# Optimization experiments

Hardware: AMD Instinct MI355X
Metric: run time of the kernel (lower is better)

## Reference

```python
import jax, jax.numpy as jnp
import numpy as np

N = 100000
E = 640000
D = 128

def setup_inputs() -> dict:
    key = jax.random.key(0)
    ks = jax.random.split(key, 12)
    s = 1.0 / np.sqrt(D)
    inp = {
        'x': jax.random.normal(ks[0], (N, D), dtype=jnp.float32),
        'edge_index': jax.random.randint(ks[1], (2, E), 0, N, dtype=jnp.int64),
    }
    names = ['W1l', 'b1', 'W1r', 'W2l', 'b2', 'W2r', 'W3l', 'b3', 'W3r']
    shapes = [(D, D), (D,), (D, D), (D, D), (D,), (D, D), (D, D), (D,), (D, D)]
    for i, (n, sh) in enumerate(zip(names, shapes)):
        inp[n] = jax.random.normal(ks[2 + i], sh, dtype=jnp.float32) * s
    return inp

def _sage_conv(x, src, dst, Wl, b, Wr):
    # mean aggregation of source features at destination nodes
    msg = x[src]                                            # [E, D] gather
    agg = jax.ops.segment_sum(msg, dst, num_segments=N)     # [N, D]
    cnt = jax.ops.segment_sum(jnp.ones((src.shape[0],), x.dtype), dst, num_segments=N)
    agg = agg / jnp.maximum(cnt, 1.0)[:, None]
    # lin_l(aggr) + lin_r(x); bias lives in lin_l (PyG default)
    return agg @ Wl.T + b + x @ Wr.T

def reference(x, edge_index, W1l, b1, W1r, W2l, b2, W2r, W3l, b3, W3r):
    src, dst = edge_index[0], edge_index[1]
    h = jax.nn.relu(_sage_conv(x, src, dst, W1l, b1, W1r))
    # dropout layers are identity in eval mode
    h = jax.nn.relu(_sage_conv(h, src, dst, W2l, b2, W2r))
    h = _sage_conv(h, src, dst, W3l, b3, W3r)
    return h
```

## Files before the change

### kernel.cpp

```cpp
#include <hip/hip_runtime.h>


typedef __attribute__((ext_vector_type(8))) short bf16x8;
typedef __attribute__((ext_vector_type(4))) float f32x4;
typedef __attribute__((ext_vector_type(4))) unsigned int u32x4;

__device__ __forceinline__ unsigned short f2bf(float f) {
  unsigned u = __float_as_uint(f);
  u += 0x7fffu + ((u >> 16) & 1u);
  return (unsigned short)(u >> 16);
}

__global__ __launch_bounds__(256) void cvt_kernel(const float* __restrict__ in,
                                                  unsigned short* __restrict__ out, int n8) {
  int i = blockIdx.x * 256 + threadIdx.x;
  if (i >= n8) return;
  const float4* p = (const float4*)(in + (size_t)i * 8);
  float4 a = p[0], b = p[1];
  union { unsigned short s[8]; u32x4 u; } pk;
  pk.s[0] = f2bf(a.x); pk.s[1] = f2bf(a.y); pk.s[2] = f2bf(a.z); pk.s[3] = f2bf(a.w);
  pk.s[4] = f2bf(b.x); pk.s[5] = f2bf(b.y); pk.s[6] = f2bf(b.z); pk.s[7] = f2bf(b.w);
  *(u32x4*)(out + (size_t)i * 8) = pk.u;
}

__global__ __launch_bounds__(256) void count_kernel(const int* __restrict__ dst,
                                                    int* __restrict__ cnt, int E, float pscale) {
  int p = blockIdx.x & 7;
  int blk = blockIdx.x >> 3;
  int stride = (gridDim.x >> 3) * 256;
  for (int e = blk * 256 + threadIdx.x; e < E; e += stride) {
    int d = dst[e];
    int pd = (int)((float)d * pscale);
    pd = pd > 7 ? 7 : pd;
    if (pd == p) atomicAdd(&cnt[d], 1);
  }
}

__global__ __launch_bounds__(256) void partial_kernel(const int* __restrict__ cnt,
                                                      int* __restrict__ blocksum, int N) {
  __shared__ int red[256];
  int t = threadIdx.x;
  int idx = blockIdx.x * 2048 + t * 8;
  int s = 0;
  if (idx + 8 <= N) {
    int4 a = *(const int4*)(cnt + idx);
    int4 b = *(const int4*)(cnt + idx + 4);
    s = a.x + a.y + a.z + a.w + b.x + b.y + b.z + b.w;
  } else {
    for (int i = idx; i < N && i < idx + 8; ++i) s += cnt[i];
  }
  red[t] = s;
  __syncthreads();
  for (int off = 128; off > 0; off >>= 1) {
    if (t < off) red[t] += red[t + off];
    __syncthreads();
  }
  if (t == 0) blocksum[blockIdx.x] = red[0];
}

__global__ __launch_bounds__(64) void scanmid_kernel(const int* __restrict__ blocksum,
                                                     int* __restrict__ blockoff, int nb) {
  int l = threadIdx.x;
  int own = (l < nb) ? blocksum[l] : 0;
  int v = own;
  for (int off = 1; off < 64; off <<= 1) {
    int u = __shfl_up(v, off);
    if (l >= off) v += u;
  }
  if (l < nb) blockoff[l] = v - own;
}

__global__ __launch_bounds__(256) void final_kernel(const int* __restrict__ cnt,
                                                    const int* __restrict__ blockoff,
                                                    int* __restrict__ rowstart,
                                                    int* __restrict__ cursor,
                                                    float* __restrict__ inv, int N) {
  __shared__ int thr[256];
  int t = threadIdx.x;
  int idx = blockIdx.x * 2048 + t * 8;
  int c[8];
  int s = 0;
#pragma unroll
  for (int i = 0; i < 8; ++i) {
    int n = idx + i;
    c[i] = (n < N) ? cnt[n] : 0;
    s += c[i];
  }
  thr[t] = s;
  __syncthreads();
  for (int off = 1; off < 256; off <<= 1) {
    int u = (t >= off) ? thr[t - off] : 0;
    __syncthreads();
    thr[t] += u;
    __syncthreads();
  }
  int run = blockoff[blockIdx.x] + thr[t] - s;
#pragma unroll
  for (int i = 0; i < 8; ++i) {
    int n = idx + i;
    if (n < N) {
      rowstart[n] = run;
      cursor[n] = run;
      inv[n] = 1.f / fmaxf((float)c[i], 1.f);
      run += c[i];
      if (n == N - 1) rowstart[N] = run;
    }
  }
}

__global__ __launch_bounds__(256) void fill_kernel(const int* __restrict__ src,
                                                   const int* __restrict__ dst,
                                                   int* __restrict__ cursor,
                                                   int* __restrict__ elist, int E, float pscale) {
  int p = blockIdx.x & 7;
  int blk = blockIdx.x >> 3;
  int stride = (gridDim.x >> 3) * 256;
  for (int e = blk * 256 + threadIdx.x; e < E; e += stride) {
    int d = dst[e];
    int s = src[e];
    int pd = (int)((float)d * pscale);
    pd = pd > 7 ? 7 : pd;
    if (pd == p) {
      int pos = atomicAdd(&cursor[d], 1);
      elist[pos] = s;
    }
  }
}

__global__ __launch_bounds__(256) void aggregate_kernel(const unsigned short* __restrict__ xbf,
                                                        const int* __restrict__ rowstart,
                                                        const int* __restrict__ elist,
                                                        const float* __restrict__ inv,
                                                        unsigned short* __restrict__ aggbf, int N) {
  int gid = blockIdx.x * 256 + threadIdx.x;
  int node = gid >> 4;
  if (node >= N) return;
  int l16 = threadIdx.x & 15;

  int beg = rowstart[node], end = rowstart[node + 1];
  float acc[8];
#pragma unroll
  for (int j = 0; j < 8; ++j) acc[j] = 0.f;

  int e = beg;
  for (; e + 2 <= end; e += 2) {
    int s0 = elist[e];
    int s1 = elist[e + 1];
    u32x4 u0 = *(const u32x4*)(xbf + ((size_t)s0 << 7) + l16 * 8);
    u32x4 u1 = *(const u32x4*)(xbf + ((size_t)s1 << 7) + l16 * 8);
#pragma unroll
    for (int d = 0; d < 4; ++d) {
      acc[2 * d]     += __uint_as_float(u0[d] << 16);
      acc[2 * d + 1] += __uint_as_float(u0[d] & 0xffff0000u);
      acc[2 * d]     += __uint_as_float(u1[d] << 16);
      acc[2 * d + 1] += __uint_as_float(u1[d] & 0xffff0000u);
    }
  }
  if (e < end) {
    int s0 = elist[e];
    u32x4 u0 = *(const u32x4*)(xbf + ((size_t)s0 << 7) + l16 * 8);
#pragma unroll
    for (int d = 0; d < 4; ++d) {
      acc[2 * d]     += __uint_as_float(u0[d] << 16);
      acc[2 * d + 1] += __uint_as_float(u0[d] & 0xffff0000u);
    }
  }

  float iv = inv[node];
  union { unsigned short s[8]; u32x4 u; } pk;
#pragma unroll
  for (int j = 0; j < 8; ++j) pk.s[j] = f2bf(acc[j] * iv);
  *(u32x4*)(aggbf + ((size_t)node << 7) + l16 * 8) = pk.u;
}

__global__ __launch_bounds__(256, 2) void sage_gemm(
    const unsigned short* __restrict__ Abf, const unsigned short* __restrict__ Xbf,
    const float* __restrict__ Wl, const float* __restrict__ Wr, const float* __restrict__ bias,
    float* __restrict__ outf, unsigned short* __restrict__ outb, int N, int relu) {
  __shared__ __align__(16) unsigned short sW[2][128][128];
  const int tid = threadIdx.x;
  for (int it = tid; it < 4096; it += 256) {
    int m = it >> 11;
    int o = (it >> 4) & 127;
    int ch = it & 15;
    const float* wsrc = (m ? Wr : Wl) + o * 128 + ch * 8;
    float4 f0 = *(const float4*)wsrc;
    float4 f1 = *(const float4*)(wsrc + 4);
    union { unsigned short s[8]; u32x4 u; } pk;
    pk.s[0] = f2bf(f0.x); pk.s[1] = f2bf(f0.y); pk.s[2] = f2bf(f0.z); pk.s[3] = f2bf(f0.w);
    pk.s[4] = f2bf(f1.x); pk.s[5] = f2bf(f1.y); pk.s[6] = f2bf(f1.z); pk.s[7] = f2bf(f1.w);
    *(u32x4*)&sW[m][o][(ch ^ (o & 15)) << 3] = pk.u;
  }
  __syncthreads();

  const int l = tid & 63;
  const int w = tid >> 6;
  const int l15 = l & 15;
  const int lg = l >> 4;
  const int row_base = blockIdx.x * 256 + w * 64;

  f32x4 acc[4][8];
#pragma unroll
  for (int rt = 0; rt < 4; ++rt)
#pragma unroll
    for (int ot = 0; ot < 8; ++ot) acc[rt][ot] = f32x4{0.f, 0.f, 0.f, 0.f};

  union frag { u32x4 u; bf16x8 v; };

  int rrow[4];
#pragma unroll
  for (int rt = 0; rt < 4; ++rt) {
    int r = row_base + rt * 16 + l15;
    rrow[rt] = (r < N) ? r : (N - 1);
  }

#pragma unroll
  for (int h = 0; h < 2; ++h) {
    const unsigned short* Asrc = h ? Xbf : Abf;
#pragma unroll
    for (int ks = 0; ks < 4; ++ks) {
      frag af[4];
#pragma unroll
      for (int rt = 0; rt < 4; ++rt)
        af[rt].u = *(const u32x4*)(Asrc + ((size_t)rrow[rt] << 7) + (ks * 32 + lg * 8));
      frag bq[8];
#pragma unroll
      for (int ot = 0; ot < 8; ++ot)
        bq[ot].u = *(const u32x4*)&sW[h][ot * 16 + l15][((((ks << 2) | lg) ^ l15)) << 3];
#pragma unroll
      for (int rt = 0; rt < 4; ++rt)
#pragma unroll
        for (int ot = 0; ot < 8; ++ot)
          acc[rt][ot] = __builtin_amdgcn_mfma_f32_16x16x32_bf16(af[rt].v, bq[ot].v, acc[rt][ot], 0, 0, 0);
    }
  }

  float bv[8];
#pragma unroll
  for (int ot = 0; ot < 8; ++ot) bv[ot] = bias[ot * 16 + l15];

#pragma unroll
  for (int rt = 0; rt < 4; ++rt) {
#pragma unroll
    for (int i = 0; i < 4; ++i) {
      int r = row_base + rt * 16 + lg * 4 + i;
      if (r < N) {
#pragma unroll
        for (int ot = 0; ot < 8; ++ot) {
          float v = acc[rt][ot][i] + bv[ot];
          if (relu) v = fmaxf(v, 0.f);
          size_t idx = ((size_t)r << 7) + ot * 16 + l15;
          if (outf) outf[idx] = v;
          else outb[idx] = f2bf(v);
        }
      }
    }
  }
}

extern "C" void kernel_launch(void* const* d_in, const int* in_sizes, int n_in,
                              void* d_out, int out_size, void* d_ws, size_t ws_size,
                              hipStream_t stream) {
  (void)n_in; (void)out_size; (void)ws_size;
  const float* x = (const float*)d_in[0];
  const int* ei = (const int*)d_in[1];
  const float* W1l = (const float*)d_in[2];
  const float* b1 = (const float*)d_in[3];
  const float* W1r = (const float*)d_in[4];
  const float* W2l = (const float*)d_in[5];
  const float* b2 = (const float*)d_in[6];
  const float* W2r = (const float*)d_in[7];
  const float* W3l = (const float*)d_in[8];
  const float* b3 = (const float*)d_in[9];
  const float* W3r = (const float*)d_in[10];
  float* out = (float*)d_out;

  const int N = in_sizes[0] / 128;
  const int E = in_sizes[1] / 2;
  const int* srcp = ei;
  const int* dstp = ei + E;
  const float pscale = 8.0f / (float)N;

  char* ws = (char*)d_ws;
  size_t off = 0;
  auto alloc = [&](size_t bytes) {
    void* p = ws + off;
    off = (off + bytes + 255) & ~(size_t)255;
    return p;
  };
  unsigned short* bufA = (unsigned short*)alloc((size_t)N * 128 * 2);
  unsigned short* bufB = (unsigned short*)alloc((size_t)N * 128 * 2);
  unsigned short* aggbf = (unsigned short*)alloc((size_t)N * 128 * 2);
  int* cnt = (int*)alloc((size_t)N * 4);
  int* rowstart = (int*)alloc((size_t)(N + 1) * 4);
  int* cursor = (int*)alloc((size_t)N * 4);
  float* inv = (float*)alloc((size_t)N * 4);
  int* elist = (int*)alloc((size_t)E * 4);
  int* blocksum = (int*)alloc(64 * 4);
  int* blockoff = (int*)alloc(64 * 4);

  const int nb = (N + 2047) / 2048;

  hipMemsetAsync(cnt, 0, (size_t)N * 4, stream);
  cvt_kernel<<<(N * 128 / 8 + 255) / 256, 256, 0, stream>>>(x, bufA, N * 128 / 8);
  count_kernel<<<1024, 256, 0, stream>>>(dstp, cnt, E, pscale);
  partial_kernel<<<nb, 256, 0, stream>>>(cnt, blocksum, N);
  scanmid_kernel<<<1, 64, 0, stream>>>(blocksum, blockoff, nb);
  final_kernel<<<nb, 256, 0, stream>>>(cnt, blockoff, rowstart, cursor, inv, N);
  fill_kernel<<<1024, 256, 0, stream>>>(srcp, dstp, cursor, elist, E, pscale);

  int aggBlocks = (N * 16 + 255) / 256;
  int gemmBlocks = (N + 255) / 256;

  aggregate_kernel<<<aggBlocks, 256, 0, stream>>>(bufA, rowstart, elist, inv, aggbf, N);
  sage_gemm<<<gemmBlocks, 256, 0, stream>>>(aggbf, bufA, W1l, W1r, b1, nullptr, bufB, N, 1);
  aggregate_kernel<<<aggBlocks, 256, 0, stream>>>(bufB, rowstart, elist, inv, aggbf, N);
  sage_gemm<<<gemmBlocks, 256, 0, stream>>>(aggbf, bufB, W2l, W2r, b2, nullptr, bufA, N, 1);
  aggregate_kernel<<<aggBlocks, 256, 0, stream>>>(bufA, rowstart, elist, inv, aggbf, N);
  sage_gemm<<<gemmBlocks, 256, 0, stream>>>(aggbf, bufA, W3l, W3r, b3, out, nullptr, N, 0);
}
```

Measured before the change: 358.4 us.

## Pre-convert weights to bf16 once and shrink GEMM tiles, reading weights from global

```diff
diff --git a/kernel.cpp b/kernel.cpp
--- a/kernel.cpp
+++ b/kernel.cpp
@@ -21,6 +21,26 @@
   pk.s[0] = f2bf(a.x); pk.s[1] = f2bf(a.y); pk.s[2] = f2bf(a.z); pk.s[3] = f2bf(a.w);
   pk.s[4] = f2bf(b.x); pk.s[5] = f2bf(b.y); pk.s[6] = f2bf(b.z); pk.s[7] = f2bf(b.w);
   *(u32x4*)(out + (size_t)i * 8) = pk.u;
+}
+
+__global__ __launch_bounds__(256) void wcvt_kernel(const float* __restrict__ w0, const float* __restrict__ w1,
+                                                   const float* __restrict__ w2, const float* __restrict__ w3,
+                                                   const float* __restrict__ w4, const float* __restrict__ w5,
+                                                   unsigned short* __restrict__ out) {
+  int i = blockIdx.x * 256 + threadIdx.x;
+  int m = i >> 11;
+  int off = (i & 2047) * 8;
+  const float* src;
+  switch (m) {
+    case 0: src = w0; break; case 1: src = w1; break; case 2: src = w2; break;
+    case 3: src = w3; break; case 4: src = w4; break; default: src = w5; break;
+  }
+  float4 a = *(const float4*)(src + off);
+  float4 b = *(const float4*)(src + off + 4);
+  union { unsigned short s[8]; u32x4 u; } pk;
+  pk.s[0] = f2bf(a.x); pk.s[1] = f2bf(a.y); pk.s[2] = f2bf(a.z); pk.s[3] = f2bf(a.w);
+  pk.s[4] = f2bf(b.x); pk.s[5] = f2bf(b.y); pk.s[6] = f2bf(b.z); pk.s[7] = f2bf(b.w);
+  *(u32x4*)(out + (size_t)m * 16384 + off) = pk.u;
 }
 
 __global__ __launch_bounds__(256) void count_kernel(const int* __restrict__ dst,
@@ -173,65 +193,43 @@
   *(u32x4*)(aggbf + ((size_t)node << 7) + l16 * 8) = pk.u;
 }
 
-__global__ __launch_bounds__(256, 2) void sage_gemm(
+__global__ __launch_bounds__(256, 4) void sage_gemm(
     const unsigned short* __restrict__ Abf, const unsigned short* __restrict__ Xbf,
-    const float* __restrict__ Wl, const float* __restrict__ Wr, const float* __restrict__ bias,
+    const unsigned short* __restrict__ Wlb, const unsigned short* __restrict__ Wrb,
+    const float* __restrict__ bias,
     float* __restrict__ outf, unsigned short* __restrict__ outb, int N, int relu) {
-  __shared__ __align__(16) unsigned short sW[2][128][128];
   const int tid = threadIdx.x;
-  for (int it = tid; it < 4096; it += 256) {
-    int m = it >> 11;
-    int o = (it >> 4) & 127;
-    int ch = it & 15;
-    const float* wsrc = (m ? Wr : Wl) + o * 128 + ch * 8;
-    float4 f0 = *(const float4*)wsrc;
-    float4 f1 = *(const float4*)(wsrc + 4);
-    union { unsigned short s[8]; u32x4 u; } pk;
-    pk.s[0] = f2bf(f0.x); pk.s[1] = f2bf(f0.y); pk.s[2] = f2bf(f0.z); pk.s[3] = f2bf(f0.w);
-    pk.s[4] = f2bf(f1.x); pk.s[5] = f2bf(f1.y); pk.s[6] = f2bf(f1.z); pk.s[7] = f2bf(f1.w);
-    *(u32x4*)&sW[m][o][(ch ^ (o & 15)) << 3] = pk.u;
-  }
-  __syncthreads();
-
   const int l = tid & 63;
   const int w = tid >> 6;
   const int l15 = l & 15;
   const int lg = l >> 4;
-  const int row_base = blockIdx.x * 256 + w * 64;
-
-  f32x4 acc[4][8];
-#pragma unroll
-  for (int rt = 0; rt < 4; ++rt)
-#pragma unroll
-    for (int ot = 0; ot < 8; ++ot) acc[rt][ot] = f32x4{0.f, 0.f, 0.f, 0.f};
+  const int row0 = blockIdx.x * 64 + w * 16;
+  if (row0 >= N) return;
+
+  int r = row0 + l15;
+  const int rrow = (r < N) ? r : (N - 1);
+
+  f32x4 acc[8];
+#pragma unroll
+  for (int ot = 0; ot < 8; ++ot) acc[ot] = f32x4{0.f, 0.f, 0.f, 0.f};
 
   union frag { u32x4 u; bf16x8 v; };
-
-  int rrow[4];
-#pragma unroll
-  for (int rt = 0; rt < 4; ++rt) {
-    int r = row_base + rt * 16 + l15;
-    rrow[rt] = (r < N) ? r : (N - 1);
-  }
 
 #pragma unroll
   for (int h = 0; h < 2; ++h) {
     const unsigned short* Asrc = h ? Xbf : Abf;
+    const unsigned short* Wsrc = h ? Wrb : Wlb;
 #pragma unroll
     for (int ks = 0; ks < 4; ++ks) {
-      frag af[4];
-#pragma unroll
-      for (int rt = 0; rt < 4; ++rt)
-        af[rt].u = *(const u32x4*)(Asrc + ((size_t)rrow[rt] << 7) + (ks * 32 + lg * 8));
+      frag af;
+      af.u = *(const u32x4*)(Asrc + ((size_t)rrow << 7) + (ks * 32 + lg * 8));
       frag bq[8];
 #pragma unroll
       for (int ot = 0; ot < 8; ++ot)
-        bq[ot].u = *(const u32x4*)&sW[h][ot * 16 + l15][((((ks << 2) | lg) ^ l15)) << 3];
-#pragma unroll
-      for (int rt = 0; rt < 4; ++rt)
-#pragma unroll
-        for (int ot = 0; ot < 8; ++ot)
-          acc[rt][ot] = __builtin_amdgcn_mfma_f32_16x16x32_bf16(af[rt].v, bq[ot].v, acc[rt][ot], 0, 0, 0);
+        bq[ot].u = *(const u32x4*)(Wsrc + (ot * 16 + l15) * 128 + (ks * 32 + lg * 8));
+#pragma unroll
+      for (int ot = 0; ot < 8; ++ot)
+        acc[ot] = __builtin_amdgcn_mfma_f32_16x16x32_bf16(af.v, bq[ot].v, acc[ot], 0, 0, 0);
     }
   }
 
@@ -240,19 +238,16 @@
   for (int ot = 0; ot < 8; ++ot) bv[ot] = bias[ot * 16 + l15];
 
 #pragma unroll
-  for (int rt = 0; rt < 4; ++rt) {
-#pragma unroll
-    for (int i = 0; i < 4; ++i) {
-      int r = row_base + rt * 16 + lg * 4 + i;
-      if (r < N) {
-#pragma unroll
-        for (int ot = 0; ot < 8; ++ot) {
-          float v = acc[rt][ot][i] + bv[ot];
-          if (relu) v = fmaxf(v, 0.f);
-          size_t idx = ((size_t)r << 7) + ot * 16 + l15;
-          if (outf) outf[idx] = v;
-          else outb[idx] = f2bf(v);
-        }
+  for (int i = 0; i < 4; ++i) {
+    int rr = row0 + lg * 4 + i;
+    if (rr < N) {
+#pragma unroll
+      for (int ot = 0; ot < 8; ++ot) {
+        float v = acc[ot][i] + bv[ot];
+        if (relu) v = fmaxf(v, 0.f);
+        size_t idx = ((size_t)rr << 7) + ot * 16 + l15;
+        if (outf) outf[idx] = v;
+        else outb[idx] = f2bf(v);
       }
     }
   }
@@ -298,24 +293,33 @@
   int* elist = (int*)alloc((size_t)E * 4);
   int* blocksum = (int*)alloc(64 * 4);
   int* blockoff = (int*)alloc(64 * 4);
+  unsigned short* wbf = (unsigned short*)alloc(6 * 16384 * 2);
 
   const int nb = (N + 2047) / 2048;
 
   hipMemsetAsync(cnt, 0, (size_t)N * 4, stream);
   cvt_kernel<<<(N * 128 / 8 + 255) / 256, 256, 0, stream>>>(x, bufA, N * 128 / 8);
+  wcvt_kernel<<<48, 256, 0, stream>>>(W1l, W1r, W2l, W2r, W3l, W3r, wbf);
   count_kernel<<<1024, 256, 0, stream>>>(dstp, cnt, E, pscale);
   partial_kernel<<<nb, 256, 0, stream>>>(cnt, blocksum, N);
   scanmid_kernel<<<1, 64, 0, stream>>>(blocksum, blockoff, nb);
   final_kernel<<<nb, 256, 0, stream>>>(cnt, blockoff, rowstart, cursor, inv, N);
   fill_kernel<<<1024, 256, 0, stream>>>(srcp, dstp, cursor, elist, E, pscale);
 
+  unsigned short* w1l = wbf;
+  unsigned short* w1r = wbf + 16384;
+  unsigned short* w2l = wbf + 2 * 16384;
+  unsigned short* w2r = wbf + 3 * 16384;
+  unsigned short* w3l = wbf + 4 * 16384;
+  unsigned short* w3r = wbf + 5 * 16384;
+
   int aggBlocks = (N * 16 + 255) / 256;
-  int gemmBlocks = (N + 255) / 256;
+  int gemmBlocks = (N + 63) / 64;
 
   aggregate_kernel<<<aggBlocks, 256, 0, stream>>>(bufA, rowstart, elist, inv, aggbf, N);
-  sage_gemm<<<gemmBlocks, 256, 0, stream>>>(aggbf, bufA, W1l, W1r, b1, nullptr, bufB, N, 1);
+  sage_gemm<<<gemmBlocks, 256, 0, stream>>>(aggbf, bufA, w1l, w1r, b1, nullptr, bufB, N, 1);
   aggregate_kernel<<<aggBlocks, 256, 0, stream>>>(bufB, rowstart, elist, inv, aggbf, N);
-  sage_gemm<<<gemmBlocks, 256, 0, stream>>>(aggbf, bufB, W2l, W2r, b2, nullptr, bufA, N, 1);
+  sage_gemm<<<gemmBlocks, 256, 0, stream>>>(aggbf, bufB, w2l, w2r, b2, nullptr, bufA, N, 1);
   aggregate_kernel<<<aggBlocks, 256, 0, stream>>>(bufA, rowstart, elist, inv, aggbf, N);
-  sage_gemm<<<gemmBlocks, 256, 0, stream>>>(aggbf, bufA, W3l, W3r, b3, out, nullptr, N, 0);
-}
+  sage_gemm<<<gemmBlocks, 256, 0, stream>>>(aggbf, bufA, w3l, w3r, b3, out, nullptr, N, 0);
+}
```

Result: slower. 472.0 us (+31.7%).
